# Performance work log

Measured on AMD Instinct MI355X. Metric: run time of the kernel, lower is better.

## Reference

```python
import jax, jax.numpy as jnp
import numpy as np

DEPTH, DIM, DH, QH, KH = 8, 512, 64, 16, 8
B, T, S = 2, 16, 257
NUM_SPECIAL, TBE, CLAMP = 1, 4, 50.0
DI = int(DIM * 4 * 2 / 3)  # 1365
EPS = 1.1920929e-07  # torch.finfo(float32).eps used by torch RMSNorm


def _rms(x, w):
    return x * jax.lax.rsqrt(jnp.mean(jnp.square(x), -1, keepdims=True) + EPS) * w


def _l2norm(x):
    return x / jnp.maximum(jnp.linalg.norm(x, axis=-1, keepdims=True), 1e-12)


def _rotary(n):
    inv = 1.0 / (10000.0 ** (jnp.arange(0, DH, 2, dtype=jnp.float32) / DH))
    f = jnp.arange(n, dtype=jnp.float32)[:, None] * inv[None, :]
    return jnp.concatenate([f, f], -1)  # [n, DH]


def _apply_rot(rot, x):
    x1, x2 = jnp.split(x, 2, -1)
    half = jnp.concatenate([-x2, x1], -1)
    return x * jnp.cos(rot) + half * jnp.sin(rot)


def _attend(q, k, v, mask=None, causal=False):
    # q: [b, QH, n, d]; k, v: [b, KH, n, d]; GQA with groups = QH//KH
    b, hq, n, d = q.shape
    h = k.shape[1]
    g = hq // h
    qg = q.reshape(b, h, g, n, d)
    sim = jnp.einsum('bhgid,bhjd->bhgij', qg, k) * (d ** -0.5)
    sim = jnp.tanh(sim / CLAMP) * CLAMP  # softclamp
    neg = -jnp.finfo(sim.dtype).max
    if mask is not None:
        sim = jnp.where(mask, sim, neg)
    if causal:
        j = sim.shape[-1]
        cm = jnp.triu(jnp.ones((n, j), bool), j - n + 1)
        sim = jnp.where(cm, neg, sim)
    attn = jax.nn.softmax(sim, axis=-1)
    out = jnp.einsum('bhgij,bhjd->bhgid', attn, v)
    return out.reshape(b, hq, n, d)


def _attn_block(x, nw, wq, wk, wv, qg, kg, wo, rot, mask, causal):
    bn, n, _ = x.shape
    h = _rms(x, nw)
    q = (h @ wq).reshape(bn, n, QH, DH).transpose(0, 2, 1, 3)
    k = (h @ wk).reshape(bn, n, KH, DH).transpose(0, 2, 1, 3)
    v = (h @ wv).reshape(bn, n, KH, DH).transpose(0, 2, 1, 3)
    sc = DH ** 0.5
    q = _l2norm(q) * ((qg + 1.0) * sc)[:, None, :]
    k = _l2norm(k) * ((kg + 1.0) * sc)[:, None, :]
    if rot is not None:
        q = _apply_rot(rot, q)
        k = _apply_rot(rot, k)
    o = _attend(q, k, v, mask=mask, causal=causal)
    o = o.transpose(0, 2, 1, 3).reshape(bn, n, QH * DH)
    return o @ wo


def _ff(x, nw, win, bin_, wout, bout):
    h = _rms(x, nw)
    a, g = jnp.split(h @ win + bin_, 2, -1)
    return (a * jax.nn.gelu(g, approximate=False)) @ wout + bout


def setup_inputs() -> dict:
    key = jax.random.key(0)
    ks = jax.random.split(key, 8)
    s = 0.02
    return {
        'tokens': jax.random.normal(ks[0], (B, T, S, DIM), jnp.float32),
        'attn_norm_w': jnp.ones((DEPTH, DIM), jnp.float32),
        'Wq': jax.random.normal(ks[1], (DEPTH, DIM, QH * DH), jnp.float32) * s,
        'Wk': jax.random.normal(ks[2], (DEPTH, DIM, KH * DH), jnp.float32) * s,
        'Wv': jax.random.normal(ks[3], (DEPTH, DIM, KH * DH), jnp.float32) * s,
        'q_gamma': jnp.zeros((DEPTH, QH, DH), jnp.float32),
        'k_gamma': jnp.zeros((DEPTH, KH, DH), jnp.float32),
        'Wo': jax.random.normal(ks[4], (DEPTH, QH * DH, DIM), jnp.float32) * s,
        'ff_norm_w': jnp.ones((DEPTH, DIM), jnp.float32),
        'W_in': jax.random.normal(ks[5], (DEPTH, DIM, 2 * DI), jnp.float32) * s,
        'b_in': jnp.zeros((DEPTH, 2 * DI), jnp.float32),
        'W_out': jax.random.normal(ks[6], (DEPTH, DI, DIM), jnp.float32) * s,
        'b_out': jnp.zeros((DEPTH, DIM), jnp.float32),
        'final_w': jnp.ones((DIM,), jnp.float32),
    }


def reference(tokens, attn_norm_w, Wq, Wk, Wv, q_gamma, k_gamma, Wo,
              ff_norm_w, W_in, b_in, W_out, b_out, final_w):
    x = tokens  # [B, T, S, D]
    # spatial special-token mask: normal tokens cannot attend to special (rightmost) tokens
    idx = jnp.arange(S)
    is_sp = idx >= (S - NUM_SPECIAL)
    sp_mask = ~((~is_sp[:, None]) & is_sp[None, :])  # [S, S]
    sp_mask = sp_mask[None, None, None]  # broadcast over (b, h, g)
    rot = _rotary(T)
    for l in range(DEPTH):
        is_time = (l + 1) % TBE == 0
        if is_time:
            y = x.transpose(0, 2, 1, 3).reshape(B * S, T, DIM)
            o = _attn_block(y, attn_norm_w[l], Wq[l], Wk[l], Wv[l], q_gamma[l],
                            k_gamma[l], Wo[l], rot=rot, mask=None, causal=True)
            x = x + o.reshape(B, S, T, DIM).transpose(0, 2, 1, 3)
        else:
            y = x.reshape(B * T, S, DIM)
            o = _attn_block(y, attn_norm_w[l], Wq[l], Wk[l], Wv[l], q_gamma[l],
                            k_gamma[l], Wo[l], rot=None, mask=sp_mask, causal=False)
            x = x + o.reshape(B, T, S, DIM)
        x = x + _ff(x, ff_norm_w[l], W_in[l], b_in[l], W_out[l], b_out[l])
    return _rms(x, final_w)
```

## Files before the change

### kernel.cpp

```cpp
#include <hip/hip_runtime.h>
#include <hip/hip_bf16.h>
#include <math.h>

typedef __attribute__((ext_vector_type(8))) short short8;
typedef __attribute__((ext_vector_type(4))) float f32x4;
typedef __hip_bfloat16 bf16;

#define BB 2
#define TT 16
#define SSQ 257
#define DIMD 512
#define NROWS 8224
#define DII 1365
#define DI2 2730
#define FNPAD 2816
#define GLULD 1408
#define SKP 288
#define EPSR 1.1920929e-07f

__device__ __forceinline__ void async16(const void* g, const void* l) {
    __builtin_amdgcn_global_load_lds(
        (const __attribute__((address_space(1))) void*)g,
        (__attribute__((address_space(3))) void*)l, 16, 0, 0);
}

__device__ __forceinline__ short f2bfs(float x) {
    bf16 h = __float2bfloat16(x);
    return *reinterpret_cast<short*>(&h);
}

__global__ void wtrans_layer(const float* __restrict__ wq, const float* __restrict__ wk,
                             const float* __restrict__ wv, const float* __restrict__ wo,
                             const float* __restrict__ win, const float* __restrict__ wout,
                             bf16* __restrict__ dqkv, bf16* __restrict__ dwo,
                             bf16* __restrict__ dwin, bf16* __restrict__ dwout) {
    __shared__ float tile[32][33];
    int bid = blockIdx.x;
    const float* src; bf16* dst; int K, M, Kpad, interleave = 0, local;
    if (bid < 512)       { src = wq;   dst = dqkv;            K = 512;  M = 1024; Kpad = 512;  local = bid; }
    else if (bid < 768)  { src = wk;   dst = dqkv + 1024*512; K = 512;  M = 512;  Kpad = 512;  local = bid - 512; }
    else if (bid < 1024) { src = wv;   dst = dqkv + 1536*512; K = 512;  M = 512;  Kpad = 512;  local = bid - 768; }
    else if (bid < 1536) { src = wo;   dst = dwo;             K = 1024; M = 512;  Kpad = 1024; local = bid - 1024; }
    else if (bid < 2944) { src = win;  dst = dwin;            K = 512;  M = 2730; Kpad = 512;  local = bid - 1536; interleave = 1; }
    else                 { src = wout; dst = dwout;           K = 1365; M = 512;  Kpad = 1408; local = bid - 2944; }
    int tilesx = Kpad >> 5;
    int k0 = (local % tilesx) * 32, m0 = (local / tilesx) * 32;
    int tx = threadIdx.x & 31, ty = threadIdx.x >> 5;
    #pragma unroll
    for (int i = 0; i < 4; ++i) {
        int k = k0 + ty + 8 * i, m = m0 + tx;
        tile[ty + 8 * i][tx] = (k < K && m < M) ? src[(size_t)k * M + m] : 0.f;
    }
    __syncthreads();
    #pragma unroll
    for (int i = 0; i < 4; ++i) {
        int n = m0 + ty + 8 * i, k = k0 + tx;
        int nd = n;
        if (interleave) nd = (n < DII) ? 2 * n : ((n < DI2) ? 2 * (n - DII) + 1 : n);
        dst[(size_t)nd * Kpad + k] = __float2bfloat16(tile[tx][ty + 8 * i]);
    }
}

template<int BF16OUT>
__global__ void rms_kernel(const float* __restrict__ x, const float* __restrict__ w,
                           void* __restrict__ out, int perm) {
    int r = blockIdx.x;
    int src = r;
    if (perm) {
        int t = r & 15; int rs = r >> 4; int s = rs % SSQ; int b = rs / SSQ;
        src = (b * TT + t) * SSQ + s;
    }
    const float* xr = x + (size_t)src * DIMD;
    int tid = threadIdx.x;
    float v0 = xr[tid], v1 = xr[tid + 256];
    __shared__ float red[256];
    red[tid] = v0 * v0 + v1 * v1;
    __syncthreads();
    for (int st = 128; st; st >>= 1) {
        if (tid < st) red[tid] += red[tid + st];
        __syncthreads();
    }
    float sc = rsqrtf(red[0] * (1.f / DIMD) + EPSR);
    if (BF16OUT) {
        bf16* o = (bf16*)out + (size_t)r * DIMD;
        o[tid] = __float2bfloat16(v0 * sc * w[tid]);
        o[tid + 256] = __float2bfloat16(v1 * sc * w[tid + 256]);
    } else {
        float* o = (float*)out + (size_t)r * DIMD;
        o[tid] = v0 * sc * w[tid];
        o[tid + 256] = v1 * sc * w[tid + 256];
    }
}

template<int EPI, int PERM, int TM>
__global__ __launch_bounds__(256)
void mfma_gemm(const bf16* __restrict__ A, int lda,
               const bf16* __restrict__ Bt, int ldb,
               const float* __restrict__ bias,
               void* __restrict__ C, int ldc, int Mstore,
               int nrow, int K,
               const float* __restrict__ qg, const float* __restrict__ kg, int rotary) {
    constexpr int MI = TM / 32;
    __shared__ __align__(16) short lds_a[2][TM * 32];
    __shared__ __align__(16) short lds_b[2][128 * 32];
    int tid = threadIdx.x;
    int wave = tid >> 6, lane = tid & 63;
    int quad = lane >> 4, l16 = lane & 15;
    int m0 = blockIdx.y * TM, n0 = blockIdx.x * 128;
    int wm = (wave & 1) * (TM / 2), wn = (wave >> 1) * 64;
    f32x4 zero4 = {0.f, 0.f, 0.f, 0.f};
    f32x4 acc[MI][4];
    #pragma unroll
    for (int i = 0; i < MI; ++i)
        #pragma unroll
        for (int j = 0; j < 4; ++j) acc[i][j] = zero4;

    const short* Ap = (const short*)A;
    const short* Bp = (const short*)Bt;
    auto aptr = [&](int g) {
        int m = g >> 2, kc = (g & 3) ^ ((g >> 3) & 3);
        int r = m0 + m; if (r >= nrow) r = nrow - 1;
        return Ap + (size_t)r * lda + kc * 8;
    };
    auto bptr = [&](int g) {
        int m = g >> 2, kc = (g & 3) ^ ((g >> 3) & 3);
        return Bp + (size_t)(n0 + m) * ldb + kc * 8;
    };
    const short* gA0; const short* gA1 = nullptr;
    int aoff0, aoff1 = 0;
    if (TM == 128) {
        gA0 = aptr(wave * 128 + lane);        aoff0 = (wave * 128) * 8;
        gA1 = aptr(wave * 128 + 64 + lane);   aoff1 = (wave * 128 + 64) * 8;
    } else {
        gA0 = aptr(wave * 64 + lane);         aoff0 = (wave * 64) * 8;
    }
    const short* gB0 = bptr(wave * 128 + lane);
    const short* gB1 = bptr(wave * 128 + 64 + lane);
    int boff0 = (wave * 128) * 8, boff1 = (wave * 128 + 64) * 8;

    auto stage = [&](int buf, int kt) {
        int ko = kt * 32;
        async16(gA0 + ko, &lds_a[buf][aoff0]);
        if (TM == 128) async16(gA1 + ko, &lds_a[buf][aoff1]);
        async16(gB0 + ko, &lds_b[buf][boff0]);
        async16(gB1 + ko, &lds_b[buf][boff1]);
    };

    int nk = K >> 5;
    stage(0, 0);
    for (int kt = 0; kt < nk; ++kt) {
        int buf = kt & 1;
        __syncthreads();
        if (kt + 1 < nk) stage(buf ^ 1, kt + 1);
        short8 af[MI], bfr[4];
        #pragma unroll
        for (int mi = 0; mi < MI; ++mi) {
            int m = wm + mi * 16 + l16;
            af[mi] = *(const short8*)&lds_a[buf][(m * 4 + (quad ^ ((m >> 1) & 3))) * 8];
        }
        #pragma unroll
        for (int nj = 0; nj < 4; ++nj) {
            int n = wn + nj * 16 + l16;
            bfr[nj] = *(const short8*)&lds_b[buf][(n * 4 + (quad ^ ((n >> 1) & 3))) * 8];
        }
        #pragma unroll
        for (int mi = 0; mi < MI; ++mi)
            #pragma unroll
            for (int nj = 0; nj < 4; ++nj)
                acc[mi][nj] = __builtin_amdgcn_mfma_f32_16x16x32_bf16(
                    af[mi], bfr[nj], acc[mi][nj], 0, 0, 0);
    }

    if constexpr (EPI == 1) {
        int head = (n0 + wn) >> 6;
        float gl0 = 0.f, gl1 = 0.f, gl2 = 0.f, gl3 = 0.f, inv0 = 0.f, inv1 = 0.f;
        if (head < 24) {
            const float* g = head < 16 ? qg + head * 64 : kg + (head - 16) * 64;
            gl0 = (g[l16] + 1.f) * 8.f;
            gl1 = (g[16 + l16] + 1.f) * 8.f;
            gl2 = (g[32 + l16] + 1.f) * 8.f;
            gl3 = (g[48 + l16] + 1.f) * 8.f;
            if (rotary) {
                inv0 = __expf(-(float)l16 * 0.28782313662425572f);
                inv1 = __expf(-(float)(l16 + 16) * 0.28782313662425572f);
            }
        }
        #pragma unroll
        for (int mi = 0; mi < MI; ++mi) {
            #pragma unroll
            for (int e = 0; e < 4; ++e) {
                int row = m0 + wm + mi * 16 + quad * 4 + e;
                float v0 = acc[mi][0][e], v1 = acc[mi][1][e];
                float v2 = acc[mi][2][e], v3 = acc[mi][3][e];
                if (head < 24) {
                    float ss = v0 * v0 + v1 * v1 + v2 * v2 + v3 * v3;
                    ss += __shfl_xor(ss, 1); ss += __shfl_xor(ss, 2);
                    ss += __shfl_xor(ss, 4); ss += __shfl_xor(ss, 8);
                    float invn = 1.f / fmaxf(sqrtf(ss), 1e-12f);
                    v0 *= invn * gl0; v1 *= invn * gl1;
                    v2 *= invn * gl2; v3 *= invn * gl3;
                    if (rotary) {
                        float t = (float)(row & 15);
                        float a0 = t * inv0, a1 = t * inv1;
                        float c0 = __cosf(a0), s0 = __sinf(a0);
                        float c1 = __cosf(a1), s1 = __sinf(a1);
                        float n0v = v0 * c0 - v2 * s0;
                        float n1v = v1 * c1 - v3 * s1;
                        float n2v = v2 * c0 + v0 * s0;
                        float n3v = v3 * c1 + v1 * s1;
                        v0 = n0v; v1 = n1v; v2 = n2v; v3 = n3v;
                    }
                }
                if (row < nrow) {
                    bf16* p = (bf16*)C + (size_t)row * ldc + n0 + wn + l16;
                    p[0]  = __float2bfloat16(v0);
                    p[16] = __float2bfloat16(v1);
                    p[32] = __float2bfloat16(v2);
                    p[48] = __float2bfloat16(v3);
                }
            }
        }
    } else if constexpr (EPI == 2) {
        #pragma unroll
        for (int mi = 0; mi < MI; ++mi) {
            #pragma unroll
            for (int e = 0; e < 4; ++e) {
                int row = m0 + wm + mi * 16 + quad * 4 + e;
                #pragma unroll
                for (int nj = 0; nj < 4; ++nj) {
                    int col = n0 + wn + nj * 16 + l16;
                    int j = col >> 1;
                    float b = (j < DII) ? ((col & 1) ? bias[DII + j] : bias[j]) : 0.f;
                    float v = acc[mi][nj][e] + b;
                    float prt = __shfl_xor(v, 1);
                    if (!(l16 & 1) && row < nrow) {
                        float gv = prt;
                        float glu = v * 0.5f * gv * (1.f + erff(gv * 0.70710678118654752f));
                        ((bf16*)C)[(size_t)row * ldc + j] = __float2bfloat16(glu);
                    }
                }
            }
        }
    } else {
        #pragma unroll
        for (int mi = 0; mi < MI; ++mi) {
            #pragma unroll
            for (int e = 0; e < 4; ++e) {
                int row = m0 + wm + mi * 16 + quad * 4 + e;
                if (row >= nrow) continue;
                int orow = row;
                if (PERM) {
                    int t = row & 15; int rs = row >> 4; int s = rs % SSQ; int b = rs / SSQ;
                    orow = (b * TT + t) * SSQ + s;
                }
                #pragma unroll
                for (int nj = 0; nj < 4; ++nj) {
                    int col = n0 + wn + nj * 16 + l16;
                    if (col >= Mstore) continue;
                    float v = acc[mi][nj][e];
                    if (bias) v += bias[col];
                    ((float*)C)[(size_t)orow * ldc + col] += v;
                }
            }
        }
    }
}

__global__ void vtrans_kernel(const bf16* __restrict__ qkv, bf16* __restrict__ vt) {
    int bkh = blockIdx.x;
    int kc = blockIdx.y;
    int bt = bkh >> 3, kh = bkh & 7;
    int tid = threadIdx.x;
    #pragma unroll
    for (int i = 0; i < 8; ++i) {
        int idx = tid + 256 * i;
        int kl = idx >> 6;
        int d = idx & 63;
        int key = kc * 32 + kl;
        float v = 0.f;
        if (key < SSQ)
            v = __bfloat162float(qkv[((size_t)(bt * SSQ + key)) * 2048 + 1536 + kh * 64 + d]);
        vt[((size_t)bkh * 64 + d) * SKP + key] = __float2bfloat16(v);
    }
}

__global__ __launch_bounds__(256)
void space_attn_kernel(const bf16* __restrict__ qkv, const bf16* __restrict__ vt,
                       bf16* __restrict__ ob) {
    __shared__ __align__(16) short kls[272 * 8 * 8];
    int qt = blockIdx.x, qh = blockIdx.y, bt = blockIdx.z;
    int kh = qh >> 1;
    int tid = threadIdx.x, wave = tid >> 6, lane = tid & 63;
    int quad = lane >> 4, l16 = lane & 15;
    int q0w = qt * 64 + wave * 16;
    int q = q0w + l16;
    int qc = q > 256 ? 256 : q;
    const short* qbase = (const short*)qkv + (size_t)bt * SSQ * 2048;

    const short* kgbase = qbase + 1024 + kh * 64;
    #pragma unroll
    for (int it = 0; it < 9; ++it) {
        int u = it * 4 + wave;
        if (u < 34) {
            int g = u * 64 + lane;
            int key = g >> 3, ch = g & 7;
            int srck = key < SSQ ? key : 256;
            async16(kgbase + (size_t)srck * 2048 + (ch ^ (key & 7)) * 8,
                    &kls[u * 512]);
        }
    }

    const short* qp = qbase + (size_t)qc * 2048 + qh * 64;
    short8 bq0 = *(const short8*)(qp + quad * 8);
    short8 bq1 = *(const short8*)(qp + 32 + quad * 8);
    __syncthreads();

    f32x4 zero4 = {0.f, 0.f, 0.f, 0.f};
    f32x4 sc[18];
    float sum = 0.f;
    int c0 = quad ^ (l16 & 7);
    #pragma unroll
    for (int kt = 0; kt < 17; ++kt) {
        int key = kt * 16 + l16;
        short8 ak0 = *(const short8*)&kls[(key * 8 + c0) * 8];
        short8 ak1 = *(const short8*)&kls[(key * 8 + (c0 ^ 4)) * 8];
        f32x4 cc = zero4;
        cc = __builtin_amdgcn_mfma_f32_16x16x32_bf16(ak0, bq0, cc, 0, 0, 0);
        cc = __builtin_amdgcn_mfma_f32_16x16x32_bf16(ak1, bq1, cc, 0, 0, 0);
        #pragma unroll
        for (int e = 0; e < 4; ++e) {
            float x = cc[e] * 0.0025f;
            float x2 = x * x;
            float v = cc[e] * 0.125f * (1.f + x2 * (-0.3333333333f + x2 * 0.1333333333f));
            float p = __expf(v);
            if (kt == 16) {
                bool valid = (e == 0) && (quad == 0) && (q == 256);
                p = valid ? p : 0.f;
            }
            cc[e] = p;
            sum += p;
        }
        sc[kt] = cc;
    }
    #pragma unroll
    for (int e = 0; e < 4; ++e) sc[17][e] = 0.f;
    sum += __shfl_xor(sum, 16);
    sum += __shfl_xor(sum, 32);
    float inv = __builtin_amdgcn_rcpf(sum);
    f32x4 inv4;
    #pragma unroll
    for (int e = 0; e < 4; ++e) inv4[e] = __shfl(inv, quad * 4 + e);

    f32x4 oacc[4];
    #pragma unroll
    for (int nt = 0; nt < 4; ++nt) oacc[nt] = zero4;
    const short* vbp = (const short*)vt + ((size_t)(bt * 8 + kh) * 64 + l16) * SKP;
    #pragma unroll
    for (int c8 = 0; c8 < 9; ++c8) {
        short8 pb;
        #pragma unroll
        for (int j = 0; j < 8; ++j) {
            int src_lane = ((quad & 1) * 2 + (j >> 2)) * 16 + l16;
            float v0 = __shfl(sc[2 * c8][j & 3], src_lane);
            float v1 = __shfl(sc[2 * c8 + 1][j & 3], src_lane);
            pb[j] = f2bfs(quad < 2 ? v0 : v1);
        }
        #pragma unroll
        for (int nt = 0; nt < 4; ++nt) {
            short8 av = *(const short8*)(vbp + (size_t)(nt * 16) * SKP + c8 * 32 + quad * 8);
            oacc[nt] = __builtin_amdgcn_mfma_f32_16x16x32_bf16(pb, av, oacc[nt], 0, 0, 0);
        }
    }

    #pragma unroll
    for (int e = 0; e < 4; ++e) {
        int qq = q0w + quad * 4 + e;
        if (qq <= 256) {
            bf16* op = ob + ((size_t)(bt * SSQ + qq)) * 1024 + qh * 64 + l16;
            float s = inv4[e];
            op[0]  = __float2bfloat16(oacc[0][e] * s);
            op[16] = __float2bfloat16(oacc[1][e] * s);
            op[32] = __float2bfloat16(oacc[2][e] * s);
            op[48] = __float2bfloat16(oacc[3][e] * s);
        }
    }
}

__global__ void time_attn_kernel(const bf16* __restrict__ qkv, bf16* __restrict__ ob) {
    __shared__ float qs[16][65], ks[16][65], ps[16][17];
    int bs = blockIdx.x, qh = blockIdx.y, kh = qh >> 1;
    int tid = threadIdx.x;
    size_t rowbase = (size_t)bs * 16;
    #pragma unroll
    for (int i = 0; i < 4; ++i) {
        int idx = tid + 256 * i;
        int r = idx >> 6, d = idx & 63;
        qs[r][d] = __bfloat162float(qkv[(rowbase + r) * 2048 + qh * 64 + d]);
        ks[r][d] = __bfloat162float(qkv[(rowbase + r) * 2048 + 1024 + kh * 64 + d]);
    }
    __syncthreads();
    int i = tid >> 4, j = tid & 15;
    float dot = 0.f;
    #pragma unroll 16
    for (int d = 0; d < 64; ++d) dot += qs[i][d] * ks[j][d];
    float s = dot * 0.125f;
    float x = s * 0.02f;
    float x2 = x * x;
    float v = s * (1.f + x2 * (-0.3333333333f + x2 * 0.1333333333f));
    float p = (j > i) ? 0.f : __expf(v);
    float sum = p;
    sum += __shfl_xor(sum, 1);
    sum += __shfl_xor(sum, 2);
    sum += __shfl_xor(sum, 4);
    sum += __shfl_xor(sum, 8);
    ps[i][j] = p * __builtin_amdgcn_rcpf(sum);
    __syncthreads();
    #pragma unroll
    for (int ii = 0; ii < 4; ++ii) {
        int idx = tid + 256 * ii;
        int r = idx >> 6, d = idx & 63;
        float acc = 0.f;
        #pragma unroll
        for (int jj = 0; jj < 16; ++jj)
            acc += ps[r][jj] * __bfloat162float(qkv[(rowbase + jj) * 2048 + 1536 + kh * 64 + d]);
        ob[(rowbase + r) * 1024 + qh * 64 + d] = __float2bfloat16(acc);
    }
}

extern "C" void kernel_launch(void* const* d_in, const int* in_sizes, int n_in,
                              void* d_out, int out_size, void* d_ws, size_t ws_size,
                              hipStream_t stream) {
    const float* tokens      = (const float*)d_in[0];
    const float* attn_norm_w = (const float*)d_in[1];
    const float* Wq          = (const float*)d_in[2];
    const float* Wk          = (const float*)d_in[3];
    const float* Wv          = (const float*)d_in[4];
    const float* q_gamma     = (const float*)d_in[5];
    const float* k_gamma     = (const float*)d_in[6];
    const float* Wo          = (const float*)d_in[7];
    const float* ff_norm_w   = (const float*)d_in[8];
    const float* W_in        = (const float*)d_in[9];
    const float* b_in        = (const float*)d_in[10];
    const float* W_out       = (const float*)d_in[11];
    const float* b_out       = (const float*)d_in[12];
    const float* final_w     = (const float*)d_in[13];

    float* x = (float*)d_out;
    char* ws = (char*)d_ws;

    bf16* wtqkv = (bf16*)ws;
    bf16* wto   = wtqkv + 2048 * 512;
    bf16* wtin  = wto   + 512 * 1024;
    bf16* wtout = wtin  + 2816 * 512;
    size_t off = (size_t)(2048*512 + 512*1024 + 2816*512 + 512*1408) * 2;
    bf16* h = (bf16*)(ws + off);
    off += (size_t)NROWS * 512 * 2;
    char* region = ws + off;
    bf16* qkv = (bf16*)region;
    bf16* glu = (bf16*)region;
    bf16* vt  = (bf16*)(region + (size_t)NROWS * 2048 * 2);
    bf16* ob  = (bf16*)(region + (size_t)NROWS * 2048 * 2 + (size_t)256*64*SKP*2);

    hipMemcpyAsync(x, tokens, (size_t)NROWS * 512 * 4, hipMemcpyDeviceToDevice, stream);

    for (int l = 0; l < 8; ++l) {
        int is_time = ((l + 1) % 4 == 0) ? 1 : 0;
        wtrans_layer<<<3648, 256, 0, stream>>>(
            Wq + (size_t)l * 512 * 1024, Wk + (size_t)l * 512 * 512,
            Wv + (size_t)l * 512 * 512, Wo + (size_t)l * 1024 * 512,
            W_in + (size_t)l * 512 * DI2, W_out + (size_t)l * DII * 512,
            wtqkv, wto, wtin, wtout);

        rms_kernel<1><<<NROWS, 256, 0, stream>>>(x, attn_norm_w + (size_t)l * 512, h, is_time);
        mfma_gemm<1, 0, 128><<<dim3(16, 65), 256, 0, stream>>>(
            h, 512, wtqkv, 512, nullptr, qkv, 2048, 2048, NROWS, 512,
            q_gamma + (size_t)l * 1024, k_gamma + (size_t)l * 512, is_time);
        if (is_time) {
            time_attn_kernel<<<dim3(514, 16), 256, 0, stream>>>(qkv, ob);
            mfma_gemm<3, 1, 64><<<dim3(4, 129), 256, 0, stream>>>(
                ob, 1024, wto, 1024, nullptr, x, 512, 512, NROWS, 1024, nullptr, nullptr, 0);
        } else {
            vtrans_kernel<<<dim3(256, 9), 256, 0, stream>>>(qkv, vt);
            space_attn_kernel<<<dim3(5, 16, 32), 256, 0, stream>>>(qkv, vt, ob);
            mfma_gemm<3, 0, 64><<<dim3(4, 129), 256, 0, stream>>>(
                ob, 1024, wto, 1024, nullptr, x, 512, 512, NROWS, 1024, nullptr, nullptr, 0);
        }

        rms_kernel<1><<<NROWS, 256, 0, stream>>>(x, ff_norm_w + (size_t)l * 512, h, 0);
        mfma_gemm<2, 0, 128><<<dim3(22, 65), 256, 0, stream>>>(
            h, 512, wtin, 512, b_in + (size_t)l * DI2, glu, GLULD, FNPAD, NROWS, 512,
            nullptr, nullptr, 0);
        mfma_gemm<3, 0, 64><<<dim3(4, 129), 256, 0, stream>>>(
            glu, GLULD, wtout, GLULD, b_out + (size_t)l * 512, x, 512, 512, NROWS, GLULD,
            nullptr, nullptr, 0);
    }

    rms_kernel<0><<<NROWS, 256, 0, stream>>>(x, final_w, x, 0);
}
```

Baseline: 2.324 ms.

## Triple-buffer GEMM LDS pipeline and use wave-per-row RMSNorm

The MFMA GEMM now keeps three LDS stages with two tiles in flight, using explicit vmcnt waits and a single barrier per k-step instead of double buffering with syncthreads. RMSNorm is rewritten so each wave processes one row with vectorised float4 loads, a shuffle reduction and a packed bf16 store, replacing the block-wide shared-memory tree reduction. The aim is to hide global-to-LDS latency and cut normalisation overhead. In exchange, LDS use per block rises and the hand-written waitcnt logic must match the number of loads per stage.

New measurement: 2.308 ms. No clear change (-0.7%).

```diff
diff --git a/kernel.cpp b/kernel.cpp
--- a/kernel.cpp
+++ b/kernel.cpp
@@ -62,33 +62,37 @@
 }
 
 template<int BF16OUT>
-__global__ void rms_kernel(const float* __restrict__ x, const float* __restrict__ w,
-                           void* __restrict__ out, int perm) {
-    int r = blockIdx.x;
+__global__ __launch_bounds__(256)
+void rms_kernel(const float* __restrict__ x, const float* __restrict__ w,
+                void* __restrict__ out, int perm) {
+    int wave = threadIdx.x >> 6, lane = threadIdx.x & 63;
+    int r = blockIdx.x * 4 + wave;
     int src = r;
     if (perm) {
         int t = r & 15; int rs = r >> 4; int s = rs % SSQ; int b = rs / SSQ;
         src = (b * TT + t) * SSQ + s;
     }
-    const float* xr = x + (size_t)src * DIMD;
-    int tid = threadIdx.x;
-    float v0 = xr[tid], v1 = xr[tid + 256];
-    __shared__ float red[256];
-    red[tid] = v0 * v0 + v1 * v1;
-    __syncthreads();
-    for (int st = 128; st; st >>= 1) {
-        if (tid < st) red[tid] += red[tid + st];
-        __syncthreads();
-    }
-    float sc = rsqrtf(red[0] * (1.f / DIMD) + EPSR);
+    const float4* xr = (const float4*)(x + (size_t)src * DIMD) + lane * 2;
+    float4 a = xr[0], c = xr[1];
+    float ss = a.x*a.x + a.y*a.y + a.z*a.z + a.w*a.w
+             + c.x*c.x + c.y*c.y + c.z*c.z + c.w*c.w;
+    ss += __shfl_xor(ss, 1);  ss += __shfl_xor(ss, 2);  ss += __shfl_xor(ss, 4);
+    ss += __shfl_xor(ss, 8);  ss += __shfl_xor(ss, 16); ss += __shfl_xor(ss, 32);
+    float sc = rsqrtf(ss * (1.f / DIMD) + EPSR);
+    const float4* wr = (const float4*)w + lane * 2;
+    float4 wa = wr[0], wb = wr[1];
     if (BF16OUT) {
-        bf16* o = (bf16*)out + (size_t)r * DIMD;
-        o[tid] = __float2bfloat16(v0 * sc * w[tid]);
-        o[tid + 256] = __float2bfloat16(v1 * sc * w[tid + 256]);
+        short8 v;
+        v[0] = f2bfs(a.x * sc * wa.x); v[1] = f2bfs(a.y * sc * wa.y);
+        v[2] = f2bfs(a.z * sc * wa.z); v[3] = f2bfs(a.w * sc * wa.w);
+        v[4] = f2bfs(c.x * sc * wb.x); v[5] = f2bfs(c.y * sc * wb.y);
+        v[6] = f2bfs(c.z * sc * wb.z); v[7] = f2bfs(c.w * sc * wb.w);
+        *(short8*)((bf16*)out + (size_t)r * DIMD + lane * 8) = v;
     } else {
-        float* o = (float*)out + (size_t)r * DIMD;
-        o[tid] = v0 * sc * w[tid];
-        o[tid + 256] = v1 * sc * w[tid + 256];
+        float4* o = (float4*)((float*)out + (size_t)r * DIMD) + lane * 2;
+        float4 o0 = {a.x * sc * wa.x, a.y * sc * wa.y, a.z * sc * wa.z, a.w * sc * wa.w};
+        float4 o1 = {c.x * sc * wb.x, c.y * sc * wb.y, c.z * sc * wb.z, c.w * sc * wb.w};
+        o[0] = o0; o[1] = o1;
     }
 }
 
@@ -101,8 +105,9 @@
                int nrow, int K,
                const float* __restrict__ qg, const float* __restrict__ kg, int rotary) {
     constexpr int MI = TM / 32;
-    __shared__ __align__(16) short lds_a[2][TM * 32];
-    __shared__ __align__(16) short lds_b[2][128 * 32];
+    constexpr int LPS = (TM == 128) ? 4 : 3;
+    __shared__ __align__(16) short lds_a[3][TM * 32];
+    __shared__ __align__(16) short lds_b[3][128 * 32];
     int tid = threadIdx.x;
     int wave = tid >> 6, lane = tid & 63;
     int quad = lane >> 4, l16 = lane & 15;
@@ -148,10 +153,21 @@
 
     int nk = K >> 5;
     stage(0, 0);
+    stage(1, 1);
+    int buf = 0;
     for (int kt = 0; kt < nk; ++kt) {
-        int buf = kt & 1;
-        __syncthreads();
-        if (kt + 1 < nk) stage(buf ^ 1, kt + 1);
+        if (kt + 1 < nk) {
+            if constexpr (LPS == 4) asm volatile("s_waitcnt vmcnt(4)" ::: "memory");
+            else                    asm volatile("s_waitcnt vmcnt(3)" ::: "memory");
+        } else {
+            asm volatile("s_waitcnt vmcnt(0)" ::: "memory");
+        }
+        __builtin_amdgcn_s_barrier();
+        __builtin_amdgcn_sched_barrier(0);
+        if (kt + 2 < nk) {
+            int nb = buf + 2; if (nb >= 3) nb -= 3;
+            stage(nb, kt + 2);
+        }
         short8 af[MI], bfr[4];
         #pragma unroll
         for (int mi = 0; mi < MI; ++mi) {
@@ -169,6 +185,7 @@
             for (int nj = 0; nj < 4; ++nj)
                 acc[mi][nj] = __builtin_amdgcn_mfma_f32_16x16x32_bf16(
                     af[mi], bfr[nj], acc[mi][nj], 0, 0, 0);
+        ++buf; if (buf >= 3) buf = 0;
     }
 
     if constexpr (EPI == 1) {
@@ -471,7 +488,7 @@
             W_in + (size_t)l * 512 * DI2, W_out + (size_t)l * DII * 512,
             wtqkv, wto, wtin, wtout);
 
-        rms_kernel<1><<<NROWS, 256, 0, stream>>>(x, attn_norm_w + (size_t)l * 512, h, is_time);
+        rms_kernel<1><<<2056, 256, 0, stream>>>(x, attn_norm_w + (size_t)l * 512, h, is_time);
         mfma_gemm<1, 0, 128><<<dim3(16, 65), 256, 0, stream>>>(
             h, 512, wtqkv, 512, nullptr, qkv, 2048, 2048, NROWS, 512,
             q_gamma + (size_t)l * 1024, k_gamma + (size_t)l * 512, is_time);
@@ -486,7 +503,7 @@
                 ob, 1024, wto, 1024, nullptr, x, 512, 512, NROWS, 1024, nullptr, nullptr, 0);
         }
 
-        rms_kernel<1><<<NROWS, 256, 0, stream>>>(x, ff_norm_w + (size_t)l * 512, h, 0);
+        rms_kernel<1><<<2056, 256, 0, stream>>>(x, ff_norm_w + (size_t)l * 512, h, 0);
         mfma_gemm<2, 0, 128><<<dim3(22, 65), 256, 0, stream>>>(
             h, 512, wtin, 512, b_in + (size_t)l * DI2, glu, GLULD, FNPAD, NROWS, 512,
             nullptr, nullptr, 0);
@@ -495,5 +512,5 @@
             nullptr, nullptr, 0);
     }
 
-    rms_kernel<0><<<NROWS, 256, 0, stream>>>(x, final_w, x, 0);
-}
+    rms_kernel<0><<<2056, 256, 0, stream>>>(x, final_w, x, 0);
+}
```
